# Kernel optimization log

Hardware: AMD Instinct MI355X
Metric: run time of the kernel (lower is better)

The kernel has to match this reference:

```python
import jax, jax.numpy as jnp
import numpy as np

KERNEL_SIZE = 128
NEG_INF = -1e30


def setup_inputs() -> dict:
    key = jax.random.key(0)
    ks = jax.random.split(key, 5)
    B, S, D, H = 4, 4096, 512, 512
    x = jax.random.normal(ks[0], (B, S, D), dtype=jnp.float32)
    # torch nn.Linear weights: [out_features, in_features], y = x @ W.T + b
    Wq_w = jax.random.normal(ks[1], (H, D), dtype=jnp.float32) * (1.0 / np.sqrt(D))
    Wq_b = jax.random.normal(ks[2], (H,), dtype=jnp.float32) * 0.01
    Wk_w = jax.random.normal(ks[3], (H, D), dtype=jnp.float32) * (1.0 / np.sqrt(D))
    Wk_b = jax.random.normal(ks[4], (H,), dtype=jnp.float32) * 0.01
    return {"x": x, "Wq_w": Wq_w, "Wq_b": Wq_b, "Wk_w": Wk_w, "Wk_b": Wk_b}


def reference(x, Wq_w, Wq_b, Wk_w, Wk_b):
    # q, k: [B, S, H]
    q = jnp.einsum('bsd,hd->bsh', x, Wq_w) + Wq_b
    k = jnp.einsum('bsd,hd->bsh', x, Wk_w) + Wk_b
    # dense scores [B, S, S]
    scores = jnp.einsum('bih,bjh->bij', q, k)
    # band mask: True where i-kernel_size+1 <= j <= i+kernel_size-1
    idx = jnp.arange(x.shape[1])
    band = jnp.abs(idx[:, None] - idx[None, :]) < KERNEL_SIZE  # [S, S]
    scores = jnp.where(band[None, :, :], scores, NEG_INF)
    attn = jax.nn.softmax(scores, axis=2)
    # attend over raw x (no V projection in original module)
    return jnp.einsum('bij,bjd->bid', attn, x)
```

## Files before the change

### kernel.cpp

```cpp
#include <hip/hip_runtime.h>
#include <hip/hip_bf16.h>

#define S_LEN 4096
#define NEG_INF_F (-1e30f)

typedef __attribute__((ext_vector_type(4))) float f32x4;
typedef __attribute__((ext_vector_type(8))) short s16x8;
typedef unsigned short u16;

static __device__ __forceinline__ u16 f2bf(float f) {
    unsigned u = __builtin_bit_cast(unsigned, f);
    unsigned r = u + 0x7FFFu + ((u >> 16) & 1u);
    return (u16)(r >> 16);
}
static __device__ __forceinline__ float bf2f(u16 h) {
    unsigned u = ((unsigned)h) << 16;
    return __builtin_bit_cast(float, u);
}
static __device__ __forceinline__ void split4(const float4 v, ushort4& hi, ushort4& lo) {
    hi.x = f2bf(v.x); lo.x = f2bf(v.x - bf2f(hi.x));
    hi.y = f2bf(v.y); lo.y = f2bf(v.y - bf2f(hi.y));
    hi.z = f2bf(v.z); lo.z = f2bf(v.z - bf2f(hi.z));
    hi.w = f2bf(v.w); lo.w = f2bf(v.w - bf2f(hi.w));
}
static __device__ __forceinline__ void gl_lds16(const void* g, void* l) {
    __builtin_amdgcn_global_load_lds(
        (const __attribute__((address_space(1))) void*)g,
        (__attribute__((address_space(3))) void*)l, 16, 0, 0);
}
static __device__ __forceinline__ int swz64(int row, int col_u16) {
    return row * 64 + (col_u16 ^ ((row & 7) << 3));
}
static __device__ __forceinline__ int swz32(int row, int col_u16) {
    return row * 32 + (col_u16 ^ (((row >> 1) & 3) << 3));
}
static __device__ __forceinline__ int swz320(int row, int col_u16) {
    return row * 320 + (col_u16 ^ ((row & 7) << 3));
}
static __device__ __forceinline__ int xcd_swz512(int bid) {
    return (bid & 7) * 64 + (bid >> 3);
}
static __device__ __forceinline__ int xcd_swz256(int bid) {
    return (bid & 7) * 32 + (bid >> 3);
}

__global__ __launch_bounds__(256) void split_xt_kernel(
    const float* __restrict__ x, u16* __restrict__ xh, u16* __restrict__ xl,
    u16* __restrict__ xT) {
    const int bid = blockIdx.x;
    const int dt = bid & 7, st = (bid >> 3) & 63, b = bid >> 9;
    const int s0 = st * 64, d0 = dt * 64;
    __shared__ u16 T[64][72];
    const int tid = threadIdx.x;
    #pragma unroll
    for (int i = 0; i < 4; ++i) {
        int idx = i * 256 + tid;
        int r = idx >> 4, c4 = (idx & 15) * 4;
        float4 v = *(const float4*)(x + (size_t)(b * S_LEN + s0 + r) * 512 + d0 + c4);
        ushort4 hi, lo; split4(v, hi, lo);
        *(ushort4*)(xh + (size_t)(b * S_LEN + s0 + r) * 512 + d0 + c4) = hi;
        *(ushort4*)(xl + (size_t)(b * S_LEN + s0 + r) * 512 + d0 + c4) = lo;
        *(ushort4*)&T[r][c4] = hi;
    }
    __syncthreads();
    #pragma unroll
    for (int i = 0; i < 2; ++i) {
        int idx = i * 256 + tid;
        int dr = idx >> 3, sc = idx & 7;
        s16x8 v;
        #pragma unroll
        for (int t = 0; t < 8; ++t) v[t] = (short)T[sc * 8 + t][dr];
        *(s16x8*)&xT[(size_t)(b * 512 + d0 + dr) * S_LEN + s0 + sc * 8] = v;
    }
}

__global__ __launch_bounds__(256) void mt_kernel(
    const float* __restrict__ Wk, const float* __restrict__ Wq,
    u16* __restrict__ Mth, u16* __restrict__ Mtl) {
    const int bm = blockIdx.x & 7, bn = blockIdx.x >> 3;
    const int m0 = bm * 64, n0 = bn * 64;
    __shared__ __align__(16) u16 Ath[64 * 72], Atl[64 * 72];
    __shared__ __align__(16) u16 Bth[64 * 72], Btl[64 * 72];
    const int tid = threadIdx.x, lane = tid & 63, w = tid >> 6;
    const int frow = lane & 15, fk = (lane >> 4) * 8;
    f32x4 acc[4] = {};

    for (int h0 = 0; h0 < 512; h0 += 64) {
        #pragma unroll
        for (int i = 0; i < 4; ++i) {
            int idx = i * 256 + tid;
            int h = idx >> 4, c4 = (idx & 15) * 4;
            float4 a = *(const float4*)(Wk + (size_t)(h0 + h) * 512 + m0 + c4);
            ushort4 ahi, alo; split4(a, ahi, alo);
            Ath[(c4 + 0) * 72 + h] = ahi.x; Atl[(c4 + 0) * 72 + h] = alo.x;
            Ath[(c4 + 1) * 72 + h] = ahi.y; Atl[(c4 + 1) * 72 + h] = alo.y;
            Ath[(c4 + 2) * 72 + h] = ahi.z; Atl[(c4 + 2) * 72 + h] = alo.z;
            Ath[(c4 + 3) * 72 + h] = ahi.w; Atl[(c4 + 3) * 72 + h] = alo.w;
            float4 b = *(const float4*)(Wq + (size_t)(h0 + h) * 512 + n0 + c4);
            ushort4 bhi, blo; split4(b, bhi, blo);
            Bth[(c4 + 0) * 72 + h] = bhi.x; Btl[(c4 + 0) * 72 + h] = blo.x;
            Bth[(c4 + 1) * 72 + h] = bhi.y; Btl[(c4 + 1) * 72 + h] = blo.y;
            Bth[(c4 + 2) * 72 + h] = bhi.z; Btl[(c4 + 2) * 72 + h] = blo.z;
            Bth[(c4 + 3) * 72 + h] = bhi.w; Btl[(c4 + 3) * 72 + h] = blo.w;
        }
        __syncthreads();
        #pragma unroll
        for (int kk = 0; kk < 2; ++kk) {
            s16x8 aH = *(const s16x8*)&Ath[(w * 16 + frow) * 72 + kk * 32 + fk];
            s16x8 aL = *(const s16x8*)&Atl[(w * 16 + frow) * 72 + kk * 32 + fk];
            #pragma unroll
            for (int ni = 0; ni < 4; ++ni) {
                s16x8 bH = *(const s16x8*)&Bth[(ni * 16 + frow) * 72 + kk * 32 + fk];
                s16x8 bL = *(const s16x8*)&Btl[(ni * 16 + frow) * 72 + kk * 32 + fk];
                acc[ni] = __builtin_amdgcn_mfma_f32_16x16x32_bf16(aH, bH, acc[ni], 0, 0, 0);
                acc[ni] = __builtin_amdgcn_mfma_f32_16x16x32_bf16(aH, bL, acc[ni], 0, 0, 0);
                acc[ni] = __builtin_amdgcn_mfma_f32_16x16x32_bf16(aL, bH, acc[ni], 0, 0, 0);
            }
        }
        __syncthreads();
    }
    #pragma unroll
    for (int ni = 0; ni < 4; ++ni) {
        int d1 = n0 + ni * 16 + frow;
        #pragma unroll
        for (int e = 0; e < 4; ++e) {
            int d2 = m0 + w * 16 + (lane >> 4) * 4 + e;
            float v = acc[ni][e];
            u16 hi = f2bf(v);
            Mth[(size_t)d2 * 512 + d1] = hi;
            Mtl[(size_t)d2 * 512 + d1] = f2bf(v - bf2f(hi));
        }
    }
}

__global__ __launch_bounds__(256) void u_kernel(
    const float* __restrict__ Wk, const float* __restrict__ bq,
    float* __restrict__ u) {
    __shared__ float red[4][64];
    const int tid = threadIdx.x, c = tid & 63, hg = tid >> 6;
    const int d2 = blockIdx.x * 64 + c;
    float acc = 0.f;
    for (int h = hg; h < 512; h += 4) acc += Wk[(size_t)h * 512 + d2] * bq[h];
    red[hg][c] = acc;
    __syncthreads();
    if (hg == 0) u[d2] = red[0][c] + red[1][c] + red[2][c] + red[3][c];
}

__global__ __launch_bounds__(512) void z_kernel(
    const u16* __restrict__ xh, const u16* __restrict__ xl,
    const u16* __restrict__ Mth, const u16* __restrict__ Mtl,
    const float* __restrict__ u, u16* __restrict__ zh, u16* __restrict__ zl) {
    const int w_ = xcd_swz512((int)blockIdx.x);
    const int bm = w_ >> 2, bn = w_ & 3;
    const int m0 = bm * 128, n0 = bn * 128;
    __shared__ __align__(16) u16 Ah[128 * 64], Al[128 * 64];
    __shared__ __align__(16) u16 Bh[128 * 64], Bl[128 * 64];
    const int tid = threadIdx.x, lane = tid & 63, w = tid >> 6;
    const int rg = w >> 2, cg = w & 3;
    const int frow = lane & 15, fk = (lane >> 4) * 8;
    f32x4 acc[4][2] = {};

    for (int k0 = 0; k0 < 512; k0 += 64) {
        #pragma unroll
        for (int i = 0; i < 2; ++i) {
            int idx = i * 512 + tid;
            int r = idx >> 3, c = idx & 7;
            int sc = (c ^ (r & 7)) * 8;
            gl_lds16(xh + (size_t)(m0 + r) * 512 + k0 + sc, &Ah[idx * 8]);
            gl_lds16(xl + (size_t)(m0 + r) * 512 + k0 + sc, &Al[idx * 8]);
            gl_lds16(Mth + (size_t)(n0 + r) * 512 + k0 + sc, &Bh[idx * 8]);
            gl_lds16(Mtl + (size_t)(n0 + r) * 512 + k0 + sc, &Bl[idx * 8]);
        }
        __syncthreads();
        #pragma unroll
        for (int kk = 0; kk < 2; ++kk) {
            s16x8 aH[4], aL[4], bH[2], bL[2];
            #pragma unroll
            for (int mi = 0; mi < 4; ++mi) {
                int row = rg * 64 + mi * 16 + frow;
                aH[mi] = *(const s16x8*)&Ah[swz64(row, kk * 32 + fk)];
                aL[mi] = *(const s16x8*)&Al[swz64(row, kk * 32 + fk)];
            }
            #pragma unroll
            for (int ni = 0; ni < 2; ++ni) {
                int row = cg * 32 + ni * 16 + frow;
                bH[ni] = *(const s16x8*)&Bh[swz64(row, kk * 32 + fk)];
                bL[ni] = *(const s16x8*)&Bl[swz64(row, kk * 32 + fk)];
            }
            #pragma unroll
            for (int mi = 0; mi < 4; ++mi)
                #pragma unroll
                for (int ni = 0; ni < 2; ++ni) {
                    acc[mi][ni] = __builtin_amdgcn_mfma_f32_16x16x32_bf16(aH[mi], bH[ni], acc[mi][ni], 0, 0, 0);
                    acc[mi][ni] = __builtin_amdgcn_mfma_f32_16x16x32_bf16(aH[mi], bL[ni], acc[mi][ni], 0, 0, 0);
                    acc[mi][ni] = __builtin_amdgcn_mfma_f32_16x16x32_bf16(aL[mi], bH[ni], acc[mi][ni], 0, 0, 0);
                }
        }
        __syncthreads();
    }
    #pragma unroll
    for (int ni = 0; ni < 2; ++ni) {
        int col = n0 + cg * 32 + ni * 16 + frow;
        float uv = u[col];
        #pragma unroll
        for (int mi = 0; mi < 4; ++mi) {
            int rbase = m0 + rg * 64 + mi * 16 + (lane >> 4) * 4;
            #pragma unroll
            for (int e = 0; e < 4; ++e) {
                float v = acc[mi][ni][e] + uv;
                u16 hi = f2bf(v);
                zh[(size_t)(rbase + e) * 512 + col] = hi;
                zl[(size_t)(rbase + e) * 512 + col] = f2bf(v - bf2f(hi));
            }
        }
    }
}

__global__ __launch_bounds__(1024, 4) void attn_kernel(
    const u16* __restrict__ zh, const u16* __restrict__ zl,
    const u16* __restrict__ xh, const u16* __restrict__ xl,
    const u16* __restrict__ xT, float* __restrict__ out) {
    const int w_ = xcd_swz256((int)blockIdx.x);
    const int b = w_ >> 6, it = w_ & 63;
    const int i0 = it * 64, j0 = i0 - 128;
    const int mrow0 = b * S_LEN + i0;

    __shared__ __align__(16) u16 smem[40960];

    const int tid = threadIdx.x, lane = tid & 63, w = tid >> 6;
    const int g = w >> 2, q = w & 3;
    const int frow = lane & 15, fk = (lane >> 4) * 8;
    const int tstart = g + q * 4;
    const int nt = (q == 3) ? 5 : 4;
    const size_t qoff = (size_t)(mrow0 + g * 16 + frow) * 512;
    const int rq = (lane >> 4) * 4;

    f32x4 acc[5] = {};
    s16x8 krA[3], krB[3];

    auto kload = [&](int s, s16x8* kr) {
        const int k0 = s * 32;
        #pragma unroll
        for (int i = 0; i < 3; ++i) {
            int f = i * 1024 + tid;
            if (f < 2560) {
                int idx = (f < 1280) ? f : f - 1280;
                int r = idx >> 2, c = idx & 3;
                int j = min(max(j0 + r, 0), S_LEN - 1);
                const u16* src = (f < 1280) ? xh : xl;
                kr[i] = *(const s16x8*)(src + (size_t)(b * S_LEN + j) * 512 + k0 + c * 8);
            }
        }
    };
    auto kwrite = [&](const s16x8* kr, int bufoff) {
        #pragma unroll
        for (int i = 0; i < 3; ++i) {
            int f = i * 1024 + tid;
            if (f < 2560) {
                int idx = (f < 1280) ? f : f - 1280;
                int r = idx >> 2, c = idx & 3;
                int off = bufoff + ((f < 1280) ? 0 : 10240) + swz32(r, c * 8);
                *(s16x8*)&smem[off] = kr[i];
            }
        }
    };
    auto qkstep = [&](int t, int bufoff) {
        const int k0 = t * 32;
        s16x8 zH = *(const s16x8*)(zh + qoff + k0 + fk);
        s16x8 zL = *(const s16x8*)(zl + qoff + k0 + fk);
        __builtin_amdgcn_s_setprio(1);
        #pragma unroll
        for (int tt = 0; tt < 5; ++tt) {
            if (tt < nt) {
                int krow = (tstart + tt) * 16 + frow;
                s16x8 bH = *(const s16x8*)&smem[bufoff + swz32(krow, fk)];
                s16x8 bL = *(const s16x8*)&smem[bufoff + 10240 + swz32(krow, fk)];
                acc[tt] = __builtin_amdgcn_mfma_f32_16x16x32_bf16(zH, bH, acc[tt], 0, 0, 0);
                acc[tt] = __builtin_amdgcn_mfma_f32_16x16x32_bf16(zH, bL, acc[tt], 0, 0, 0);
                acc[tt] = __builtin_amdgcn_mfma_f32_16x16x32_bf16(zL, bH, acc[tt], 0, 0, 0);
            }
        }
        __builtin_amdgcn_s_setprio(0);
    };

    kload(0, krA);
    kwrite(krA, 0);
    kload(1, krB);
    __syncthreads();
    for (int tt2 = 0; tt2 < 16; tt2 += 2) {
        if (tt2 + 1 < 16) kwrite(krB, 20480);
        if (tt2 + 2 < 16) kload(tt2 + 2, krA);
        qkstep(tt2, 0);
        __syncthreads();
        if (tt2 + 1 < 16) {
            if (tt2 + 2 < 16) kwrite(krA, 0);
            if (tt2 + 3 < 16) kload(tt2 + 3, krB);
            qkstep(tt2 + 1, 20480);
            __syncthreads();
        }
    }

    float* sred_max = (float*)&smem[20480];
    float* sred_sum = sred_max + 256;
    #pragma unroll
    for (int e = 0; e < 4; ++e) {
        int r = g * 16 + rq + e;
        float m = NEG_INF_F;
        #pragma unroll
        for (int tt = 0; tt < 5; ++tt) {
            if (tt < nt) {
                int jj = (tstart + tt) * 16 + frow;
                int dj = jj - r, j = j0 + jj;
                if (dj >= 1 && dj <= 255 && j >= 0 && j < S_LEN) m = fmaxf(m, acc[tt][e]);
            }
        }
        #pragma unroll
        for (int d = 1; d < 16; d <<= 1) m = fmaxf(m, __shfl_xor(m, d));
        if (frow == 0) sred_max[r * 4 + q] = m;
    }
    __syncthreads();
    float sh[4];
    #pragma unroll
    for (int e = 0; e < 4; ++e) {
        int r = g * 16 + rq + e;
        float mx = fmaxf(fmaxf(sred_max[r * 4], sred_max[r * 4 + 1]),
                         fmaxf(sred_max[r * 4 + 2], sred_max[r * 4 + 3]));
        float s = 0.f;
        #pragma unroll
        for (int tt = 0; tt < 5; ++tt) {
            float pv = 0.f;
            if (tt < nt) {
                int jj = (tstart + tt) * 16 + frow;
                int dj = jj - r, j = j0 + jj;
                bool valid = (dj >= 1 && dj <= 255 && j >= 0 && j < S_LEN);
                pv = valid ? __expf(acc[tt][e] - mx) : 0.f;
            }
            acc[tt][e] = pv;
            s += pv;
        }
        #pragma unroll
        for (int d = 1; d < 16; d <<= 1) s += __shfl_xor(s, d);
        sh[e] = s;
    }
    if (frow == 0) {
        #pragma unroll
        for (int e = 0; e < 4; ++e) sred_sum[(g * 16 + rq + e) * 4 + q] = sh[e];
    }
    __syncthreads();
    float invv[4];
    #pragma unroll
    for (int e = 0; e < 4; ++e) {
        int r = g * 16 + rq + e;
        invv[e] = 1.f / (sred_sum[r * 4] + sred_sum[r * 4 + 1] +
                         sred_sum[r * 4 + 2] + sred_sum[r * 4 + 3]);
    }
    __syncthreads();
    #pragma unroll
    for (int tt = 0; tt < 5; ++tt) {
        if (tt < nt) {
            int t = tstart + tt;
            #pragma unroll
            for (int e = 0; e < 4; ++e) {
                int r = g * 16 + rq + e;
                smem[swz320(r, t * 16 + frow)] = f2bf(acc[tt][e] * invv[e]);
            }
        }
    }
    if (q == 0) {
        for (int t = 0; t < g; ++t)
            #pragma unroll
            for (int e = 0; e < 4; ++e)
                smem[swz320(g * 16 + rq + e, t * 16 + frow)] = 0;
    }
    if (q == 3) {
        for (int t = g + 17; t < 20; ++t)
            #pragma unroll
            for (int e = 0; e < 4; ++e)
                smem[swz320(g * 16 + rq + e, t * 16 + frow)] = 0;
    }

    s16x8 vreg[3];
    auto vload = [&](int ds) {
        const int d0 = ds * 64;
        #pragma unroll
        for (int i = 0; i < 3; ++i) {
            int f = i * 1024 + tid;
            if (f < 2560) {
                int dr = f / 40, c8 = f - dr * 40;
                int jb = j0 + c8 * 8;
                jb = min(max(jb, 0), S_LEN - 8);
                vreg[i] = *(const s16x8*)&xT[(size_t)(b * 512 + d0 + dr) * S_LEN + jb];
            }
        }
    };
    auto vwrite = [&]() {
        #pragma unroll
        for (int i = 0; i < 3; ++i) {
            int f = i * 1024 + tid;
            if (f < 2560) {
                int dr = f / 40, c8 = f - dr * 40;
                *(s16x8*)&smem[20480 + swz320(dr, c8 * 8)] = vreg[i];
            }
        }
    };
    vload(0);
    for (int ds = 0; ds < 8; ++ds) {
        __syncthreads();
        vwrite();
        __syncthreads();
        if (ds < 7) vload(ds + 1);
        f32x4 po = {};
        __builtin_amdgcn_s_setprio(1);
        #pragma unroll
        for (int jt = 0; jt < 10; ++jt) {
            s16x8 a = *(const s16x8*)&smem[swz320(g * 16 + frow, jt * 32 + fk)];
            s16x8 bv = *(const s16x8*)&smem[20480 + swz320(q * 16 + frow, jt * 32 + fk)];
            po = __builtin_amdgcn_mfma_f32_16x16x32_bf16(a, bv, po, 0, 0, 0);
        }
        __builtin_amdgcn_s_setprio(0);
        #pragma unroll
        for (int e = 0; e < 4; ++e) {
            int r = mrow0 + g * 16 + rq + e;
            out[(size_t)r * 512 + ds * 64 + q * 16 + frow] = po[e];
        }
    }
}

extern "C" void kernel_launch(void* const* d_in, const int* in_sizes, int n_in,
                              void* d_out, int out_size, void* d_ws, size_t ws_size,
                              hipStream_t stream) {
    const float* x  = (const float*)d_in[0];
    const float* Wq = (const float*)d_in[1];
    const float* bq = (const float*)d_in[2];
    const float* Wk = (const float*)d_in[3];
    const float* bk = (const float*)d_in[4];
    (void)bk;
    float* out = (float*)d_out;

    u16* xh  = (u16*)d_ws;
    u16* xl  = xh + (size_t)8388608;
    u16* zh  = xl + (size_t)8388608;
    u16* zl  = zh + (size_t)8388608;
    u16* Mth = zl + (size_t)8388608;
    u16* Mtl = Mth + (size_t)262144;
    u16* xT  = Mtl + (size_t)262144;
    float* uv = (float*)(xT + (size_t)8388608);

    hipLaunchKernelGGL(split_xt_kernel, dim3(2048), dim3(256), 0, stream, x, xh, xl, xT);
    hipLaunchKernelGGL(mt_kernel, dim3(64), dim3(256), 0, stream, Wk, Wq, Mth, Mtl);
    hipLaunchKernelGGL(u_kernel, dim3(8), dim3(256), 0, stream, Wk, bq, uv);
    hipLaunchKernelGGL(z_kernel, dim3(512), dim3(512), 0, stream,
                       xh, xl, Mth, Mtl, uv, zh, zl);
    hipLaunchKernelGGL(attn_kernel, dim3(256), dim3(1024), 0, stream,
                       zh, zl, xh, xl, xT, out);
}
```

Before: 137.2 us.

## Remap QK warps to two row-groups each and cache P fragments in registers

The QK phase now assigns each warp two 16-row query groups and a 2-3 key tile slice, so each key fragment read from shared memory feeds six MFMAs instead of three. This halves LDS reads of K per MFMA and balances tiles across 8 warps per row pair. The softmax reductions are widened to 8 partials per row. In the PV phase the probability A-fragments are loaded once into registers before the d-loop rather than reloaded each iteration, at the cost of more VGPRs under the 1024-thread, 4-wave launch bound, which may cause spills.

After: 155.0 us. 13.0% more time.

```diff
diff --git a/kernel.cpp b/kernel.cpp
--- a/kernel.cpp
+++ b/kernel.cpp
@@ -228,14 +228,17 @@
     __shared__ __align__(16) u16 smem[40960];
 
     const int tid = threadIdx.x, lane = tid & 63, w = tid >> 6;
-    const int g = w >> 2, q = w & 3;
     const int frow = lane & 15, fk = (lane >> 4) * 8;
-    const int tstart = g + q * 4;
-    const int nt = (q == 3) ? 5 : 4;
-    const size_t qoff = (size_t)(mrow0 + g * 16 + frow) * 512;
     const int rq = (lane >> 4) * 4;
 
-    f32x4 acc[5] = {};
+    const int rgp = w >> 3, q8 = w & 7;
+    const int tstart_rel = (q8 < 6) ? 2 * q8 : 12 + (q8 - 6) * 3;
+    const int ntq = (q8 < 6) ? 2 : 3;
+    const int tbase = 2 * rgp + tstart_rel;
+    const size_t qoff0 = (size_t)(mrow0 + (2 * rgp + 0) * 16 + frow) * 512;
+    const size_t qoff1 = (size_t)(mrow0 + (2 * rgp + 1) * 16 + frow) * 512;
+
+    f32x4 acc[2][3] = {};
     s16x8 krA[3], krB[3];
 
     auto kload = [&](int s, s16x8* kr) {
@@ -266,18 +269,23 @@
     };
     auto qkstep = [&](int t, int bufoff) {
         const int k0 = t * 32;
-        s16x8 zH = *(const s16x8*)(zh + qoff + k0 + fk);
-        s16x8 zL = *(const s16x8*)(zl + qoff + k0 + fk);
+        s16x8 zH0 = *(const s16x8*)(zh + qoff0 + k0 + fk);
+        s16x8 zL0 = *(const s16x8*)(zl + qoff0 + k0 + fk);
+        s16x8 zH1 = *(const s16x8*)(zh + qoff1 + k0 + fk);
+        s16x8 zL1 = *(const s16x8*)(zl + qoff1 + k0 + fk);
         __builtin_amdgcn_s_setprio(1);
         #pragma unroll
-        for (int tt = 0; tt < 5; ++tt) {
-            if (tt < nt) {
-                int krow = (tstart + tt) * 16 + frow;
+        for (int tt = 0; tt < 3; ++tt) {
+            if (tt < ntq) {
+                int krow = (tbase + tt) * 16 + frow;
                 s16x8 bH = *(const s16x8*)&smem[bufoff + swz32(krow, fk)];
                 s16x8 bL = *(const s16x8*)&smem[bufoff + 10240 + swz32(krow, fk)];
-                acc[tt] = __builtin_amdgcn_mfma_f32_16x16x32_bf16(zH, bH, acc[tt], 0, 0, 0);
-                acc[tt] = __builtin_amdgcn_mfma_f32_16x16x32_bf16(zH, bL, acc[tt], 0, 0, 0);
-                acc[tt] = __builtin_amdgcn_mfma_f32_16x16x32_bf16(zL, bH, acc[tt], 0, 0, 0);
+                acc[0][tt] = __builtin_amdgcn_mfma_f32_16x16x32_bf16(zH0, bH, acc[0][tt], 0, 0, 0);
+                acc[0][tt] = __builtin_amdgcn_mfma_f32_16x16x32_bf16(zH0, bL, acc[0][tt], 0, 0, 0);
+                acc[0][tt] = __builtin_amdgcn_mfma_f32_16x16x32_bf16(zL0, bH, acc[0][tt], 0, 0, 0);
+                acc[1][tt] = __builtin_amdgcn_mfma_f32_16x16x32_bf16(zH1, bH, acc[1][tt], 0, 0, 0);
+                acc[1][tt] = __builtin_amdgcn_mfma_f32_16x16x32_bf16(zH1, bL, acc[1][tt], 0, 0, 0);
+                acc[1][tt] = __builtin_amdgcn_mfma_f32_16x16x32_bf16(zL1, bH, acc[1][tt], 0, 0, 0);
             }
         }
         __builtin_amdgcn_s_setprio(0);
@@ -301,83 +309,108 @@
     }
 
     float* sred_max = (float*)&smem[20480];
-    float* sred_sum = sred_max + 256;
-    #pragma unroll
-    for (int e = 0; e < 4; ++e) {
-        int r = g * 16 + rq + e;
-        float m = NEG_INF_F;
-        #pragma unroll
-        for (int tt = 0; tt < 5; ++tt) {
-            if (tt < nt) {
-                int jj = (tstart + tt) * 16 + frow;
-                int dj = jj - r, j = j0 + jj;
-                if (dj >= 1 && dj <= 255 && j >= 0 && j < S_LEN) m = fmaxf(m, acc[tt][e]);
-            }
-        }
-        #pragma unroll
-        for (int d = 1; d < 16; d <<= 1) m = fmaxf(m, __shfl_xor(m, d));
-        if (frow == 0) sred_max[r * 4 + q] = m;
-    }
-    __syncthreads();
-    float sh[4];
-    #pragma unroll
-    for (int e = 0; e < 4; ++e) {
-        int r = g * 16 + rq + e;
-        float mx = fmaxf(fmaxf(sred_max[r * 4], sred_max[r * 4 + 1]),
-                         fmaxf(sred_max[r * 4 + 2], sred_max[r * 4 + 3]));
-        float s = 0.f;
-        #pragma unroll
-        for (int tt = 0; tt < 5; ++tt) {
-            float pv = 0.f;
-            if (tt < nt) {
-                int jj = (tstart + tt) * 16 + frow;
-                int dj = jj - r, j = j0 + jj;
-                bool valid = (dj >= 1 && dj <= 255 && j >= 0 && j < S_LEN);
-                pv = valid ? __expf(acc[tt][e] - mx) : 0.f;
-            }
-            acc[tt][e] = pv;
-            s += pv;
-        }
-        #pragma unroll
-        for (int d = 1; d < 16; d <<= 1) s += __shfl_xor(s, d);
-        sh[e] = s;
+    float* sred_sum = sred_max + 512;
+    #pragma unroll
+    for (int sub = 0; sub < 2; ++sub) {
+        #pragma unroll
+        for (int e = 0; e < 4; ++e) {
+            int r = (2 * rgp + sub) * 16 + rq + e;
+            float m = NEG_INF_F;
+            #pragma unroll
+            for (int tt = 0; tt < 3; ++tt) {
+                if (tt < ntq) {
+                    int jj = (tbase + tt) * 16 + frow;
+                    int dj = jj - r, j = j0 + jj;
+                    if (dj >= 1 && dj <= 255 && j >= 0 && j < S_LEN) m = fmaxf(m, acc[sub][tt][e]);
+                }
+            }
+            #pragma unroll
+            for (int d = 1; d < 16; d <<= 1) m = fmaxf(m, __shfl_xor(m, d));
+            if (frow == 0) sred_max[r * 8 + q8] = m;
+        }
+    }
+    __syncthreads();
+    float sh[2][4];
+    #pragma unroll
+    for (int sub = 0; sub < 2; ++sub) {
+        #pragma unroll
+        for (int e = 0; e < 4; ++e) {
+            int r = (2 * rgp + sub) * 16 + rq + e;
+            float mx = NEG_INF_F;
+            #pragma unroll
+            for (int k = 0; k < 8; ++k) mx = fmaxf(mx, sred_max[r * 8 + k]);
+            float s = 0.f;
+            #pragma unroll
+            for (int tt = 0; tt < 3; ++tt) {
+                float pv = 0.f;
+                if (tt < ntq) {
+                    int jj = (tbase + tt) * 16 + frow;
+                    int dj = jj - r, j = j0 + jj;
+                    bool valid = (dj >= 1 && dj <= 255 && j >= 0 && j < S_LEN);
+                    pv = valid ? __expf(acc[sub][tt][e] - mx) : 0.f;
+                }
+                acc[sub][tt][e] = pv;
+                s += pv;
+            }
+            #pragma unroll
+            for (int d = 1; d < 16; d <<= 1) s += __shfl_xor(s, d);
+            sh[sub][e] = s;
+        }
     }
     if (frow == 0) {
         #pragma unroll
-        for (int e = 0; e < 4; ++e) sred_sum[(g * 16 + rq + e) * 4 + q] = sh[e];
-    }
-    __syncthreads();
-    float invv[4];
-    #pragma unroll
-    for (int e = 0; e < 4; ++e) {
-        int r = g * 16 + rq + e;
-        invv[e] = 1.f / (sred_sum[r * 4] + sred_sum[r * 4 + 1] +
-                         sred_sum[r * 4 + 2] + sred_sum[r * 4 + 3]);
-    }
-    __syncthreads();
-    #pragma unroll
-    for (int tt = 0; tt < 5; ++tt) {
-        if (tt < nt) {
-            int t = tstart + tt;
-            #pragma unroll
-            for (int e = 0; e < 4; ++e) {
-                int r = g * 16 + rq + e;
-                smem[swz320(r, t * 16 + frow)] = f2bf(acc[tt][e] * invv[e]);
-            }
-        }
-    }
-    if (q == 0) {
-        for (int t = 0; t < g; ++t)
+        for (int sub = 0; sub < 2; ++sub)
             #pragma unroll
             for (int e = 0; e < 4; ++e)
-                smem[swz320(g * 16 + rq + e, t * 16 + frow)] = 0;
-    }
-    if (q == 3) {
-        for (int t = g + 17; t < 20; ++t)
-            #pragma unroll
-            for (int e = 0; e < 4; ++e)
-                smem[swz320(g * 16 + rq + e, t * 16 + frow)] = 0;
-    }
+                sred_sum[((2 * rgp + sub) * 16 + rq + e) * 8 + q8] = sh[sub][e];
+    }
+    __syncthreads();
+    float invv[2][4];
+    #pragma unroll
+    for (int sub = 0; sub < 2; ++sub) {
+        #pragma unroll
+        for (int e = 0; e < 4; ++e) {
+            int r = (2 * rgp + sub) * 16 + rq + e;
+            float s = 0.f;
+            #pragma unroll
+            for (int k = 0; k < 8; ++k) s += sred_sum[r * 8 + k];
+            invv[sub][e] = 1.f / s;
+        }
+    }
+    __syncthreads();
+    #pragma unroll
+    for (int sub = 0; sub < 2; ++sub) {
+        #pragma unroll
+        for (int tt = 0; tt < 3; ++tt) {
+            if (tt < ntq) {
+                int t = tbase + tt;
+                #pragma unroll
+                for (int e = 0; e < 4; ++e) {
+                    int r = (2 * rgp + sub) * 16 + rq + e;
+                    smem[swz320(r, t * 16 + frow)] = f2bf(acc[sub][tt][e] * invv[sub][e]);
+                }
+            }
+        }
+    }
+    if (q8 == 0) {
+        #pragma unroll
+        for (int t2 = 0; t2 < 2; ++t2) {
+            int t = rgp ? t2 : 18 + t2;
+            #pragma unroll
+            for (int sub = 0; sub < 2; ++sub)
+                #pragma unroll
+                for (int e = 0; e < 4; ++e)
+                    smem[swz320(rgp * 32 + sub * 16 + rq + e, t * 16 + frow)] = 0;
+        }
+    }
+    __syncthreads();
+
+    const int g = w >> 2, qd = w & 3;
+
+    s16x8 afrag[10];
+    #pragma unroll
+    for (int jt = 0; jt < 10; ++jt)
+        afrag[jt] = *(const s16x8*)&smem[swz320(g * 16 + frow, jt * 32 + fk)];
 
     s16x8 vreg[3];
     auto vload = [&](int ds) {
@@ -413,15 +446,14 @@
         __builtin_amdgcn_s_setprio(1);
         #pragma unroll
         for (int jt = 0; jt < 10; ++jt) {
-            s16x8 a = *(const s16x8*)&smem[swz320(g * 16 + frow, jt * 32 + fk)];
-            s16x8 bv = *(const s16x8*)&smem[20480 + swz320(q * 16 + frow, jt * 32 + fk)];
-            po = __builtin_amdgcn_mfma_f32_16x16x32_bf16(a, bv, po, 0, 0, 0);
+            s16x8 bv = *(const s16x8*)&smem[20480 + swz320(qd * 16 + frow, jt * 32 + fk)];
+            po = __builtin_amdgcn_mfma_f32_16x16x32_bf16(afrag[jt], bv, po, 0, 0, 0);
         }
         __builtin_amdgcn_s_setprio(0);
         #pragma unroll
         for (int e = 0; e < 4; ++e) {
             int r = mrow0 + g * 16 + rq + e;
-            out[(size_t)r * 512 + ds * 64 + q * 16 + frow] = po[e];
+            out[(size_t)r * 512 + ds * 64 + qd * 16 + frow] = po[e];
         }
     }
 }
```

## Prefetch next K-tile into registers to overlap global loads with MFMA in z_kernel

Applied to the files above, without the earlier changes.

Replaces the direct global-to-LDS loads in z_kernel with a register-staged software pipeline. The next K-tile is loaded into registers while MFMAs run on the current tile, then written into swizzled LDS at the start of the next iteration. It also raises wave priority around the MFMA block and adds a min-blocks launch bound. In exchange it adds register pressure (eight 16-byte staging registers per thread) and an extra LDS write pass, and the launch-bound hint may force spills.

Result: slower. 147.3 us (+7.4%).

```diff
diff --git a/kernel.cpp b/kernel.cpp
--- a/kernel.cpp
+++ b/kernel.cpp
@@ -146,7 +146,7 @@
     if (hg == 0) u[d2] = red[0][c] + red[1][c] + red[2][c] + red[3][c];
 }
 
-__global__ __launch_bounds__(512) void z_kernel(
+__global__ __launch_bounds__(512, 4) void z_kernel(
     const u16* __restrict__ xh, const u16* __restrict__ xl,
     const u16* __restrict__ Mth, const u16* __restrict__ Mtl,
     const float* __restrict__ u, u16* __restrict__ zh, u16* __restrict__ zl) {
@@ -159,19 +159,37 @@
     const int rg = w >> 2, cg = w & 3;
     const int frow = lane & 15, fk = (lane >> 4) * 8;
     f32x4 acc[4][2] = {};
-
-    for (int k0 = 0; k0 < 512; k0 += 64) {
-        #pragma unroll
-        for (int i = 0; i < 2; ++i) {
-            int idx = i * 512 + tid;
+    s16x8 zr[8];
+
+    auto kload = [&](int t) {
+        const int k0 = t * 64;
+        #pragma unroll
+        for (int i = 0; i < 8; ++i) {
+            int f = i * 512 + tid;
+            int idx = f & 1023;
             int r = idx >> 3, c = idx & 7;
-            int sc = (c ^ (r & 7)) * 8;
-            gl_lds16(xh + (size_t)(m0 + r) * 512 + k0 + sc, &Ah[idx * 8]);
-            gl_lds16(xl + (size_t)(m0 + r) * 512 + k0 + sc, &Al[idx * 8]);
-            gl_lds16(Mth + (size_t)(n0 + r) * 512 + k0 + sc, &Bh[idx * 8]);
-            gl_lds16(Mtl + (size_t)(n0 + r) * 512 + k0 + sc, &Bl[idx * 8]);
-        }
-        __syncthreads();
+            const u16* src = (f < 1024) ? xh : (f < 2048) ? xl : (f < 3072) ? Mth : Mtl;
+            const int row0 = (f < 2048) ? m0 : n0;
+            zr[i] = *(const s16x8*)(src + (size_t)(row0 + r) * 512 + k0 + c * 8);
+        }
+    };
+    auto kwrite = [&]() {
+        #pragma unroll
+        for (int i = 0; i < 8; ++i) {
+            int f = i * 512 + tid;
+            int idx = f & 1023;
+            int r = idx >> 3, c = idx & 7;
+            u16* dst = (f < 1024) ? Ah : (f < 2048) ? Al : (f < 3072) ? Bh : Bl;
+            *(s16x8*)&dst[swz64(r, c * 8)] = zr[i];
+        }
+    };
+
+    kload(0);
+    for (int t = 0; t < 8; ++t) {
+        __syncthreads();
+        kwrite();
+        __syncthreads();
+        if (t < 7) kload(t + 1);
         #pragma unroll
         for (int kk = 0; kk < 2; ++kk) {
             s16x8 aH[4], aL[4], bH[2], bL[2];
@@ -187,6 +205,7 @@
                 bH[ni] = *(const s16x8*)&Bh[swz64(row, kk * 32 + fk)];
                 bL[ni] = *(const s16x8*)&Bl[swz64(row, kk * 32 + fk)];
             }
+            __builtin_amdgcn_s_setprio(1);
             #pragma unroll
             for (int mi = 0; mi < 4; ++mi)
                 #pragma unroll
@@ -195,8 +214,8 @@
                     acc[mi][ni] = __builtin_amdgcn_mfma_f32_16x16x32_bf16(aH[mi], bL[ni], acc[mi][ni], 0, 0, 0);
                     acc[mi][ni] = __builtin_amdgcn_mfma_f32_16x16x32_bf16(aL[mi], bH[ni], acc[mi][ni], 0, 0, 0);
                 }
-        }
-        __syncthreads();
+            __builtin_amdgcn_s_setprio(0);
+        }
     }
     #pragma unroll
     for (int ni = 0; ni < 2; ++ni) {
```
